# Kernel optimization log

Measured on AMD Instinct MI355X. Metric: run time of the kernel, lower is better.

The kernel has to match this reference:

```python
import jax, jax.numpy as jnp
import numpy as np

NEG_INF = -9e15
NEG_SLOPE = 0.2

def setup_inputs() -> dict:
    key = jax.random.key(0)
    k1, k2, k3, k4 = jax.random.split(key, 4)
    N, d_in, d_out = 8192, 256, 256
    x = jax.random.normal(k1, (N, d_in), dtype=jnp.float32)
    adj = jax.random.randint(k2, (N, N), 0, 2).astype(jnp.float32)
    W = jax.random.normal(k3, (d_in, d_out), dtype=jnp.float32) * (1.0 / np.sqrt(d_in))
    a = jax.random.normal(k4, (2 * d_out,), dtype=jnp.float32) * (1.0 / np.sqrt(2 * d_out))
    return {"x": x, "adj": adj, "W": W, "a": a}

def reference(x, adj, W, a):
    d_out = W.shape[1]
    Wh = x @ W                                   # [N, d_out]
    # a([Wh_i || Wh_j]) decomposed: e_ij = <a_src, Wh_i> + <a_dst, Wh_j>
    e_src = Wh @ a[:d_out]                       # [N]
    e_dst = Wh @ a[d_out:]                       # [N]
    e = jax.nn.leaky_relu(e_src[:, None] + e_dst[None, :], NEG_SLOPE)  # [N, N]
    N = Wh.shape[0]
    mask = (adj > 0) | jnp.eye(N, dtype=bool)
    e = jnp.where(mask, e, NEG_INF)
    alpha = jax.nn.softmax(e, axis=1)            # [N, N]
    h = alpha @ Wh                               # [N, d_out]
    return h
```

## Files before the change

kernel.cpp:

```cpp
#include <hip/hip_runtime.h>
#include <stdint.h>

#define N 8192
#define D 256

typedef __attribute__((ext_vector_type(4))) float f32x4;
typedef __attribute__((ext_vector_type(8))) short bf16x8;

__device__ __forceinline__ unsigned short f2bf(float f) {
    unsigned u = __float_as_uint(f);
    u += 0x7fff + ((u >> 16) & 1);
    return (unsigned short)(u >> 16);
}
__device__ __forceinline__ float leaky(float x) {
    return fmaxf(x, 0.f) + 0.2f * fminf(x, 0.f);
}
__device__ __forceinline__ void sync_lds() {
    asm volatile("s_waitcnt lgkmcnt(0)\n\ts_barrier" ::: "memory");
}

#define K1_BM 16
__global__ __launch_bounds__(256) void k1_gemm(const float* __restrict__ x,
                                               const float* __restrict__ W,
                                               float* __restrict__ Wh,
                                               unsigned short* __restrict__ WhT) {
    __shared__ float xsT[32][20];
    const int t = threadIdx.x;
    const int r0 = blockIdx.x * K1_BM;
    float acc[K1_BM];
#pragma unroll
    for (int i = 0; i < K1_BM; ++i) acc[i] = 0.f;

    for (int k0 = 0; k0 < D; k0 += 32) {
        __syncthreads();
        if (t < 128) {
            int r = t >> 3, ks = (t & 7) * 4;
            float4 v = *(const float4*)(x + (size_t)(r0 + r) * D + k0 + ks);
            xsT[ks + 0][r] = v.x; xsT[ks + 1][r] = v.y;
            xsT[ks + 2][r] = v.z; xsT[ks + 3][r] = v.w;
        }
        __syncthreads();
#pragma unroll 8
        for (int kk = 0; kk < 32; ++kk) {
            float wv = W[(size_t)(k0 + kk) * D + t];
#pragma unroll
            for (int rc = 0; rc < K1_BM / 4; ++rc) {
                float4 xv = *(const float4*)&xsT[kk][rc * 4];
                acc[rc * 4 + 0] += xv.x * wv;
                acc[rc * 4 + 1] += xv.y * wv;
                acc[rc * 4 + 2] += xv.z * wv;
                acc[rc * 4 + 3] += xv.w * wv;
            }
        }
    }
#pragma unroll
    for (int r = 0; r < K1_BM; ++r) Wh[(size_t)(r0 + r) * D + t] = acc[r];
    unsigned short pk[K1_BM];
#pragma unroll
    for (int r = 0; r < K1_BM; ++r) pk[r] = f2bf(acc[r]);
    uint4* dst = (uint4*)(WhT + (size_t)t * N + r0);
    dst[0] = *(uint4*)&pk[0];
    dst[1] = *(uint4*)&pk[8];
}

__global__ __launch_bounds__(256) void k2_edot(const float* __restrict__ Wh,
                                               const float* __restrict__ a,
                                               float* __restrict__ e_src,
                                               float* __restrict__ e_dst) {
    const int wave = threadIdx.x >> 6, lane = threadIdx.x & 63;
    const int row = blockIdx.x * 4 + wave;
    float4 wv = *(const float4*)(Wh + (size_t)row * D + lane * 4);
    float4 as = *(const float4*)(a + lane * 4);
    float4 ad = *(const float4*)(a + D + lane * 4);
    float ps = wv.x * as.x + wv.y * as.y + wv.z * as.z + wv.w * as.w;
    float pd = wv.x * ad.x + wv.y * ad.y + wv.z * ad.z + wv.w * ad.w;
#pragma unroll
    for (int m = 1; m < 64; m <<= 1) {
        ps += __shfl_xor(ps, m);
        pd += __shfl_xor(pd, m);
    }
    if (lane == 0) { e_src[row] = ps; e_dst[row] = pd; }
}

__global__ __launch_bounds__(256) void k3_max(const float* __restrict__ e_dst,
                                              float* __restrict__ maxdst) {
    __shared__ float red[4];
    const int t = threadIdx.x;
    float m = -3.4e38f;
    for (int i = t; i < N; i += 256) m = fmaxf(m, e_dst[i]);
#pragma unroll
    for (int msk = 1; msk < 64; msk <<= 1) m = fmaxf(m, __shfl_xor(m, msk));
    if ((t & 63) == 0) red[t >> 6] = m;
    __syncthreads();
    if (t == 0) *maxdst = fmaxf(fmaxf(red[0], red[1]), fmaxf(red[2], red[3]));
}

#define BM 64
#define BK 64
#define RB (N / BM)
#define SPLITS 8
#define NITER ((N / SPLITS) / BK)
#define PSTRIDE 72
__global__ __launch_bounds__(512, 4) void k4_main(const float* __restrict__ adj,
                                                  const unsigned short* __restrict__ WhT,
                                                  const float* __restrict__ e_src,
                                                  const float* __restrict__ e_dst,
                                                  const float* __restrict__ maxdst,
                                                  float* __restrict__ O_part,
                                                  float* __restrict__ l_part) {
    __shared__ unsigned short p_lds[2][BM][PSTRIDE];

    const int t = threadIdx.x;
    const int rb = blockIdx.x & (RB - 1);
    const int s  = blockIdx.x >> 7;
    const int r0 = rb * BM;
    const int j0 = s * (N / SPLITS);

    const int pr = t >> 3;
    const int pc = (t & 7) * 8;
    const int gr = r0 + pr;

    const int w = t >> 6;
    const int lane = t & 63;
    const int quad = lane >> 4, lo = lane & 15;

    const float md = *maxdst;
    const float es = e_src[gr];
    const float m = leaky(es + md);

    f32x4 acc[4][2];
#pragma unroll
    for (int mt = 0; mt < 4; ++mt)
#pragma unroll
        for (int nt = 0; nt < 2; ++nt)
            acc[mt][nt] = (f32x4){0.f, 0.f, 0.f, 0.f};
    float lsum = 0.f;

    const float* adj_row = adj + (size_t)gr * N + j0 + pc;
    const float* ed_row  = e_dst + j0 + pc;
    const unsigned short* wt_base = WhT + (size_t)(w * 32 + lo) * N + j0 + quad * 8;

    float4 adjv0, adjv1, edv0, edv1;
    bf16x8 bfr[2][2];

    adjv0 = *(const float4*)(adj_row);
    adjv1 = *(const float4*)(adj_row + 4);
    edv0  = *(const float4*)(ed_row);
    edv1  = *(const float4*)(ed_row + 4);
#pragma unroll
    for (int ks2 = 0; ks2 < 2; ++ks2)
#pragma unroll
        for (int nt = 0; nt < 2; ++nt)
            bfr[ks2][nt] = *(const bf16x8*)(wt_base + (size_t)nt * (16 * N) + ks2 * 32);

    auto stage = [&](int its, int buf) {
        const int jb = j0 + its * BK + pc;
        float av[8] = {adjv0.x, adjv0.y, adjv0.z, adjv0.w,
                       adjv1.x, adjv1.y, adjv1.z, adjv1.w};
        float ev[8] = {edv0.x, edv0.y, edv0.z, edv0.w,
                       edv1.x, edv1.y, edv1.z, edv1.w};
        unsigned short pk[8];
#pragma unroll
        for (int jj = 0; jj < 8; ++jj) {
            float e = leaky(es + ev[jj]);
            bool keep = (av[jj] > 0.f) || (jb + jj == gr);
            float p = keep ? __expf(e - m) : 0.f;
            lsum += p;
            pk[jj] = f2bf(p);
        }
        *(uint4*)&p_lds[buf][pr][pc] = *(uint4*)pk;
    };

    stage(0, 0);
    adjv0 = *(const float4*)(adj_row + BK);
    adjv1 = *(const float4*)(adj_row + BK + 4);
    edv0  = *(const float4*)(ed_row + BK);
    edv1  = *(const float4*)(ed_row + BK + 4);
    sync_lds();

#pragma unroll 2
    for (int it = 0; it < NITER; ++it) {
        const int cb = it & 1, nb = cb ^ 1;

#pragma unroll
        for (int ks2 = 0; ks2 < 2; ++ks2) {
            bf16x8 afr[4];
#pragma unroll
            for (int mt = 0; mt < 4; ++mt)
                afr[mt] = *(const bf16x8*)&p_lds[cb][mt * 16 + lo][ks2 * 32 + quad * 8];
#pragma unroll
            for (int nt = 0; nt < 2; ++nt)
#pragma unroll
                for (int mt = 0; mt < 4; ++mt)
                    acc[mt][nt] = __builtin_amdgcn_mfma_f32_16x16x32_bf16(
                        afr[mt], bfr[ks2][nt], acc[mt][nt], 0, 0, 0);
        }

        {
            const int itn = (it + 1 < NITER) ? it + 1 : NITER - 1;
#pragma unroll
            for (int ks2 = 0; ks2 < 2; ++ks2)
#pragma unroll
                for (int nt = 0; nt < 2; ++nt)
                    bfr[ks2][nt] = *(const bf16x8*)(wt_base + (size_t)nt * (16 * N) +
                                                    itn * BK + ks2 * 32);
        }

        if (it + 1 < NITER) {
            stage(it + 1, nb);
            const int itn2 = (it + 2 < NITER) ? it + 2 : NITER - 1;
            adjv0 = *(const float4*)(adj_row + itn2 * BK);
            adjv1 = *(const float4*)(adj_row + itn2 * BK + 4);
            edv0  = *(const float4*)(ed_row + itn2 * BK);
            edv1  = *(const float4*)(ed_row + itn2 * BK + 4);
        }
        sync_lds();
    }

#pragma unroll
    for (int msk = 1; msk < 8; msk <<= 1) lsum += __shfl_xor(lsum, msk);
    if ((t & 7) == 0) l_part[(size_t)s * N + gr] = lsum;

#pragma unroll
    for (int mt = 0; mt < 4; ++mt) {
#pragma unroll
        for (int nt = 0; nt < 2; ++nt) {
            f32x4 v = acc[mt][nt];
            int col = w * 32 + nt * 16 + lo;
#pragma unroll
            for (int reg = 0; reg < 4; ++reg) {
                int row = mt * 16 + quad * 4 + reg;
                O_part[((size_t)s * N + r0 + row) * D + col] = v[reg];
            }
        }
    }
}

__global__ __launch_bounds__(256) void k5_reduce(const float* __restrict__ O_part,
                                                 const float* __restrict__ l_part,
                                                 float* __restrict__ out) {
    const int idx = blockIdx.x * 256 + threadIdx.x;
    const int r = idx >> 6;
    float lsum = 0.f;
#pragma unroll
    for (int s = 0; s < SPLITS; ++s) lsum += l_part[(size_t)s * N + r];
    f32x4 o = (f32x4){0.f, 0.f, 0.f, 0.f};
#pragma unroll
    for (int s = 0; s < SPLITS; ++s)
        o += *(const f32x4*)(O_part + (size_t)s * N * D + (size_t)idx * 4);
    const float inv = 1.f / lsum;
    *(f32x4*)(out + (size_t)idx * 4) = o * inv;
}

extern "C" void kernel_launch(void* const* d_in, const int* in_sizes, int n_in,
                              void* d_out, int out_size, void* d_ws, size_t ws_size,
                              hipStream_t stream) {
    const float* x   = (const float*)d_in[0];
    const float* adj = (const float*)d_in[1];
    const float* W   = (const float*)d_in[2];
    const float* a   = (const float*)d_in[3];
    float* out = (float*)d_out;

    char* ws = (char*)d_ws;
    float* Wh            = (float*)(ws);
    unsigned short* WhT  = (unsigned short*)(ws + 8388608);
    float* e_src         = (float*)(ws + 12582912);
    float* e_dst         = (float*)(ws + 12615680);
    float* maxdst        = (float*)(ws + 12648448);
    float* l_part        = (float*)(ws + 12648704);
    float* O_part        = (float*)(ws + 16777216);

    k1_gemm<<<N / K1_BM, 256, 0, stream>>>(x, W, Wh, WhT);
    k2_edot<<<N / 4, 256, 0, stream>>>(Wh, a, e_src, e_dst);
    k3_max<<<1, 256, 0, stream>>>(e_dst, maxdst);
    k4_main<<<RB * SPLITS, 512, 0, stream>>>(adj, WhT, e_src, e_dst, maxdst, O_part, l_part);
    k5_reduce<<<N * D / 4 / 256, 256, 0, stream>>>(O_part, l_part, out);
}
```

Before: 485.4 us.

## Deepen adj prefetch to two tiles, reorder split-major blocks, raise occupancy hint

```diff
diff --git a/kernel.cpp b/kernel.cpp
--- a/kernel.cpp
+++ b/kernel.cpp
@@ -31,25 +31,29 @@
 #pragma unroll
     for (int i = 0; i < K1_BM; ++i) acc[i] = 0.f;
 
+    const int lr = t >> 3, lks = (t & 7) * 4;
+    float4 xv;
+    if (t < 128) xv = *(const float4*)(x + (size_t)(r0 + lr) * D + lks);
+
     for (int k0 = 0; k0 < D; k0 += 32) {
         __syncthreads();
         if (t < 128) {
-            int r = t >> 3, ks = (t & 7) * 4;
-            float4 v = *(const float4*)(x + (size_t)(r0 + r) * D + k0 + ks);
-            xsT[ks + 0][r] = v.x; xsT[ks + 1][r] = v.y;
-            xsT[ks + 2][r] = v.z; xsT[ks + 3][r] = v.w;
+            xsT[lks + 0][lr] = xv.x; xsT[lks + 1][lr] = xv.y;
+            xsT[lks + 2][lr] = xv.z; xsT[lks + 3][lr] = xv.w;
         }
         __syncthreads();
+        if (t < 128 && k0 + 32 < D)
+            xv = *(const float4*)(x + (size_t)(r0 + lr) * D + k0 + 32 + lks);
 #pragma unroll 8
         for (int kk = 0; kk < 32; ++kk) {
             float wv = W[(size_t)(k0 + kk) * D + t];
 #pragma unroll
             for (int rc = 0; rc < K1_BM / 4; ++rc) {
-                float4 xv = *(const float4*)&xsT[kk][rc * 4];
-                acc[rc * 4 + 0] += xv.x * wv;
-                acc[rc * 4 + 1] += xv.y * wv;
-                acc[rc * 4 + 2] += xv.z * wv;
-                acc[rc * 4 + 3] += xv.w * wv;
+                float4 xr = *(const float4*)&xsT[kk][rc * 4];
+                acc[rc * 4 + 0] += xr.x * wv;
+                acc[rc * 4 + 1] += xr.y * wv;
+                acc[rc * 4 + 2] += xr.z * wv;
+                acc[rc * 4 + 3] += xr.w * wv;
             }
         }
     }
@@ -101,7 +105,7 @@
 #define SPLITS 8
 #define NITER ((N / SPLITS) / BK)
 #define PSTRIDE 72
-__global__ __launch_bounds__(512, 4) void k4_main(const float* __restrict__ adj,
+__global__ __launch_bounds__(512, 8) void k4_main(const float* __restrict__ adj,
                                                   const unsigned short* __restrict__ WhT,
                                                   const float* __restrict__ e_src,
                                                   const float* __restrict__ e_dst,
@@ -111,8 +115,8 @@
     __shared__ unsigned short p_lds[2][BM][PSTRIDE];
 
     const int t = threadIdx.x;
-    const int rb = blockIdx.x & (RB - 1);
-    const int s  = blockIdx.x >> 7;
+    const int rb = blockIdx.x >> 3;
+    const int s  = blockIdx.x & 7;
     const int r0 = rb * BM;
     const int j0 = s * (N / SPLITS);
 
@@ -140,25 +144,38 @@
     const float* ed_row  = e_dst + j0 + pc;
     const unsigned short* wt_base = WhT + (size_t)(w * 32 + lo) * N + j0 + quad * 8;
 
-    float4 adjv0, adjv1, edv0, edv1;
+    float4 aA0, aA1;
+    float4 aB0, aB1;
+    float4 edv0, edv1;
     bf16x8 bfr[2][2];
 
-    adjv0 = *(const float4*)(adj_row);
-    adjv1 = *(const float4*)(adj_row + 4);
-    edv0  = *(const float4*)(ed_row);
-    edv1  = *(const float4*)(ed_row + 4);
-#pragma unroll
-    for (int ks2 = 0; ks2 < 2; ++ks2)
-#pragma unroll
-        for (int nt = 0; nt < 2; ++nt)
-            bfr[ks2][nt] = *(const bf16x8*)(wt_base + (size_t)nt * (16 * N) + ks2 * 32);
-
-    auto stage = [&](int its, int buf) {
+    auto mma = [&](int cb) {
+#pragma unroll
+        for (int ks2 = 0; ks2 < 2; ++ks2) {
+            bf16x8 afr[4];
+#pragma unroll
+            for (int mt = 0; mt < 4; ++mt)
+                afr[mt] = *(const bf16x8*)&p_lds[cb][mt * 16 + lo][ks2 * 32 + quad * 8];
+#pragma unroll
+            for (int nt = 0; nt < 2; ++nt)
+#pragma unroll
+                for (int mt = 0; mt < 4; ++mt)
+                    acc[mt][nt] = __builtin_amdgcn_mfma_f32_16x16x32_bf16(
+                        afr[mt], bfr[ks2][nt], acc[mt][nt], 0, 0, 0);
+        }
+    };
+    auto bfr_load = [&](int it) {
+#pragma unroll
+        for (int ks2 = 0; ks2 < 2; ++ks2)
+#pragma unroll
+            for (int nt = 0; nt < 2; ++nt)
+                bfr[ks2][nt] = *(const bf16x8*)(wt_base + (size_t)nt * (16 * N) +
+                                                it * BK + ks2 * 32);
+    };
+    auto stage = [&](int its, int buf, float4 a0, float4 a1, float4 e0, float4 e1) {
         const int jb = j0 + its * BK + pc;
-        float av[8] = {adjv0.x, adjv0.y, adjv0.z, adjv0.w,
-                       adjv1.x, adjv1.y, adjv1.z, adjv1.w};
-        float ev[8] = {edv0.x, edv0.y, edv0.z, edv0.w,
-                       edv1.x, edv1.y, edv1.z, edv1.w};
+        float av[8] = {a0.x, a0.y, a0.z, a0.w, a1.x, a1.y, a1.z, a1.w};
+        float ev[8] = {e0.x, e0.y, e0.z, e0.w, e1.x, e1.y, e1.z, e1.w};
         unsigned short pk[8];
 #pragma unroll
         for (int jj = 0; jj < 8; ++jj) {
@@ -171,50 +188,50 @@
         *(uint4*)&p_lds[buf][pr][pc] = *(uint4*)pk;
     };
 
-    stage(0, 0);
-    adjv0 = *(const float4*)(adj_row + BK);
-    adjv1 = *(const float4*)(adj_row + BK + 4);
-    edv0  = *(const float4*)(ed_row + BK);
-    edv1  = *(const float4*)(ed_row + BK + 4);
+    aA0 = *(const float4*)(adj_row);
+    aA1 = *(const float4*)(adj_row + 4);
+    aB0 = *(const float4*)(adj_row + BK);
+    aB1 = *(const float4*)(adj_row + BK + 4);
+    edv0 = *(const float4*)(ed_row);
+    edv1 = *(const float4*)(ed_row + 4);
+    bfr_load(0);
+    stage(0, 0, aA0, aA1, edv0, edv1);
+    edv0 = *(const float4*)(ed_row + BK);
+    edv1 = *(const float4*)(ed_row + BK + 4);
+    aA0 = *(const float4*)(adj_row + 2 * BK);
+    aA1 = *(const float4*)(adj_row + 2 * BK + 4);
     sync_lds();
 
-#pragma unroll 2
-    for (int it = 0; it < NITER; ++it) {
-        const int cb = it & 1, nb = cb ^ 1;
-
-#pragma unroll
-        for (int ks2 = 0; ks2 < 2; ++ks2) {
-            bf16x8 afr[4];
-#pragma unroll
-            for (int mt = 0; mt < 4; ++mt)
-                afr[mt] = *(const bf16x8*)&p_lds[cb][mt * 16 + lo][ks2 * 32 + quad * 8];
-#pragma unroll
-            for (int nt = 0; nt < 2; ++nt)
-#pragma unroll
-                for (int mt = 0; mt < 4; ++mt)
-                    acc[mt][nt] = __builtin_amdgcn_mfma_f32_16x16x32_bf16(
-                        afr[mt], bfr[ks2][nt], acc[mt][nt], 0, 0, 0);
-        }
-
+    for (int it2 = 0; it2 < NITER / 2; ++it2) {
         {
-            const int itn = (it + 1 < NITER) ? it + 1 : NITER - 1;
-#pragma unroll
-            for (int ks2 = 0; ks2 < 2; ++ks2)
-#pragma unroll
-                for (int nt = 0; nt < 2; ++nt)
-                    bfr[ks2][nt] = *(const bf16x8*)(wt_base + (size_t)nt * (16 * N) +
-                                                    itn * BK + ks2 * 32);
-        }
-
-        if (it + 1 < NITER) {
-            stage(it + 1, nb);
-            const int itn2 = (it + 2 < NITER) ? it + 2 : NITER - 1;
-            adjv0 = *(const float4*)(adj_row + itn2 * BK);
-            adjv1 = *(const float4*)(adj_row + itn2 * BK + 4);
-            edv0  = *(const float4*)(ed_row + itn2 * BK);
-            edv1  = *(const float4*)(ed_row + itn2 * BK + 4);
-        }
-        sync_lds();
+            const int it = it2 * 2;
+            mma(0);
+            bfr_load(it + 1);
+            stage(it + 1, 1, aB0, aB1, edv0, edv1);
+            const int itn = (it + 2 < NITER) ? it + 2 : NITER - 1;
+            edv0 = *(const float4*)(ed_row + itn * BK);
+            edv1 = *(const float4*)(ed_row + itn * BK + 4);
+            const int itn3 = (it + 3 < NITER) ? it + 3 : NITER - 1;
+            aB0 = *(const float4*)(adj_row + itn3 * BK);
+            aB1 = *(const float4*)(adj_row + itn3 * BK + 4);
+            sync_lds();
+        }
+        {
+            const int it = it2 * 2 + 1;
+            mma(1);
+            const int itb = (it + 1 < NITER) ? it + 1 : NITER - 1;
+            bfr_load(itb);
+            if (it + 1 < NITER) {
+                stage(it + 1, 0, aA0, aA1, edv0, edv1);
+                const int itn = (it + 2 < NITER) ? it + 2 : NITER - 1;
+                edv0 = *(const float4*)(ed_row + itn * BK);
+                edv1 = *(const float4*)(ed_row + itn * BK + 4);
+                const int itn3 = (it + 3 < NITER) ? it + 3 : NITER - 1;
+                aA0 = *(const float4*)(adj_row + itn3 * BK);
+                aA1 = *(const float4*)(adj_row + itn3 * BK + 4);
+            }
+            sync_lds();
+        }
     }
 
 #pragma unroll
```

After: 1.019 ms. 110% more time.
